# Optimization experiments

Measured on AMD Instinct MI355X. Metric: run time of the kernel, lower is better.

Reference implementation:

```python
import jax, jax.numpy as jnp
import numpy as np

N, E, KS, DIM = 6890, 41340, 5, 2
K = KS * KS  # 25 spline kernel buckets


def spline_conv(x, edge_index, pseudo, weight, root, bias):
    """Degree-1 open B-spline conv (SplineGCN), mean aggregation + root + bias.
    x: [N, Fin], weight: [K, Fin, Fout], root: [Fin, Fout], bias: [Fout]."""
    row, col = edge_index[0], edge_index[1]  # target, source
    pos = pseudo * (KS - 1)                   # [E, 2] in [0, KS-1]
    i0 = jnp.clip(jnp.floor(pos), 0, KS - 2).astype(jnp.int32)  # [E, 2]
    frac = pos - i0                           # [E, 2]
    # 4 nonzero basis products per edge (2 per dim)
    off = jnp.array([[0, 0], [1, 0], [0, 1], [1, 1]], dtype=jnp.int32)  # [4, 2]
    b_dim = jnp.stack([1.0 - frac, frac], axis=-1)  # [E, 2, 2] (dim, which-knot)
    w = b_dim[:, 0, off[:, 0]] * b_dim[:, 1, off[:, 1]]       # [E, 4]
    idx = (i0[:, None, 0] + off[None, :, 0]) + KS * (i0[:, None, 1] + off[None, :, 1])  # [E, 4]
    # transform all nodes by all K kernels once: [N, K, Fout]
    xw = jnp.einsum('ni,kio->nko', x, weight)
    g = xw[col[:, None], idx]                 # [E, 4, Fout] gather
    msg = jnp.einsum('es,eso->eo', w, g)      # [E, Fout]
    agg = jax.ops.segment_sum(msg, row, num_segments=N)
    deg = jax.ops.segment_sum(jnp.ones((E,), x.dtype), row, num_segments=N)
    agg = agg / jnp.maximum(deg, 1.0)[:, None]
    return agg + x @ root + bias


def setup_inputs() -> dict:
    key = jax.random.key(0)
    ks = jax.random.split(key, 20)
    def gl(k, shape):  # glorot-ish
        fan = shape[-2] if len(shape) > 1 else shape[-1]
        return jax.random.normal(k, shape, jnp.float32) / np.sqrt(fan)
    inp = {
        'x': jax.random.normal(ks[0], (N, 544), jnp.float32),
        'edge_index': jax.random.randint(ks[1], (2, E), 0, N),
        'pseudo': jax.random.uniform(ks[2], (E, DIM), jnp.float32),
        'W_lin': gl(ks[3], (544, 16)), 'b_lin': jnp.zeros((16,), jnp.float32),
        'w1': gl(ks[4], (K, 16, 32)),  'r1': gl(ks[5], (16, 32)),  'bi1': jnp.zeros((32,), jnp.float32),
        'w2': gl(ks[6], (K, 32, 64)),  'r2': gl(ks[7], (32, 64)),  'bi2': jnp.zeros((64,), jnp.float32),
        'w3': gl(ks[8], (K, 64, 128)), 'r3': gl(ks[9], (64, 128)), 'bi3': jnp.zeros((128,), jnp.float32),
        'W1': gl(ks[10], (128, 256)), 'b1': jnp.zeros((256,), jnp.float32),
        'W2': gl(ks[11], (256, 6890)), 'b2': jnp.zeros((6890,), jnp.float32),
    }
    return inp


def reference(x, edge_index, pseudo, W_lin, b_lin, w1, r1, bi1, w2, r2, bi2, w3, r3, bi3, W1, b1, W2, b2):
    h = jax.nn.elu(x @ W_lin + b_lin)
    h = jax.nn.elu(spline_conv(h, edge_index, pseudo, w1, r1, bi1))
    h = jax.nn.elu(spline_conv(h, edge_index, pseudo, w2, r2, bi2))
    h = jax.nn.elu(spline_conv(h, edge_index, pseudo, w3, r3, bi3))
    h = jax.nn.elu(h @ W1 + b1)
    # dropout is identity in eval mode
    logits = h @ W2 + b2
    return jax.nn.log_softmax(logits, axis=-1)
```

## Files before the change

### kernel.cpp

```cpp
#include <hip/hip_runtime.h>
#include <hip/hip_bf16.h>

#define NND 6890
#define NED 41340

typedef __bf16 bf16x8 __attribute__((ext_vector_type(8)));
typedef float f32x4 __attribute__((ext_vector_type(4)));
typedef unsigned short u16x4 __attribute__((ext_vector_type(4)));

__device__ inline unsigned short f32_bf16(float f) {
  unsigned int u = __float_as_uint(f);
  unsigned int r = (u + 0x7FFFu + ((u >> 16) & 1u)) >> 16;
  return (unsigned short)r;
}
__device__ inline void split2(float v, unsigned short& hi, unsigned short& lo) {
  unsigned short h = f32_bf16(v);
  float hf = __uint_as_float((unsigned int)h << 16);
  hi = h;
  lo = f32_bf16(v - hf);
}
__device__ inline float elu_f(float v) { return v > 0.f ? v : (expf(v) - 1.f); }

__device__ __forceinline__ void gload_lds16(const void* g, void* l) {
  __builtin_amdgcn_global_load_lds((const __attribute__((address_space(1))) void*)g,
                                   (__attribute__((address_space(3))) void*)l, 16, 0, 0);
}

__global__ void zero_int_kernel(int* p, int n) {
  int i = blockIdx.x * blockDim.x + threadIdx.x;
  if (i < n) p[i] = 0;
}

__global__ void edge_prep_kernel(const int* __restrict__ erow, const float* __restrict__ pseudo,
                                 float* __restrict__ ew, int* __restrict__ ek,
                                 int* __restrict__ deg, int E) {
  int e = blockIdx.x * blockDim.x + threadIdx.x;
  if (e >= E) return;
  float p0 = pseudo[2 * e + 0] * 4.0f;
  float p1 = pseudo[2 * e + 1] * 4.0f;
  int i0 = (int)floorf(p0); i0 = i0 < 0 ? 0 : (i0 > 3 ? 3 : i0);
  int i1 = (int)floorf(p1); i1 = i1 < 0 ? 0 : (i1 > 3 ? 3 : i1);
  float f0 = p0 - (float)i0, f1 = p1 - (float)i1;
  ew[4 * e + 0] = (1.f - f0) * (1.f - f1);
  ew[4 * e + 1] = f0 * (1.f - f1);
  ew[4 * e + 2] = (1.f - f0) * f1;
  ew[4 * e + 3] = f0 * f1;
  int b = i0 + 5 * i1;
  ek[4 * e + 0] = b; ek[4 * e + 1] = b + 1; ek[4 * e + 2] = b + 5; ek[4 * e + 3] = b + 6;
  atomicAdd(&deg[erow[e]], 1);
}

__global__ void scan_kernel(const int* __restrict__ deg, int* __restrict__ rowptr,
                            int* __restrict__ cursor, float* __restrict__ deginv, int n) {
  __shared__ int part[1024];
  int t = threadIdx.x;
  int CH = (n + 1023) >> 10;
  int base = t * CH;
  int s = 0;
  for (int j = 0; j < CH; ++j) { int i = base + j; if (i < n) s += deg[i]; }
  part[t] = s;
  __syncthreads();
  for (int off = 1; off < 1024; off <<= 1) {
    int v = (t >= off) ? part[t - off] : 0;
    __syncthreads();
    part[t] += v;
    __syncthreads();
  }
  int run = (t == 0) ? 0 : part[t - 1];
  for (int j = 0; j < CH; ++j) {
    int i = base + j;
    if (i < n) {
      rowptr[i] = run; cursor[i] = run;
      int d = deg[i];
      deginv[i] = 1.0f / fmaxf((float)d, 1.0f);
      run += d;
    }
  }
  if (t == 1023) rowptr[n] = part[1023];
}

__global__ void csr_fill_kernel(const int* __restrict__ erow, int* __restrict__ cursor,
                                int* __restrict__ csr, int E) {
  int e = blockIdx.x * blockDim.x + threadIdx.x;
  if (e >= E) return;
  int slot = atomicAdd(&cursor[erow[e]], 1);
  csr[slot] = e;
}

__global__ void split_kernel(const float* __restrict__ src, unsigned short* __restrict__ oh,
                             unsigned short* __restrict__ ol, int n4) {
  int i = blockIdx.x * 256 + threadIdx.x;
  if (i >= n4) return;
  f32x4 v = *(const f32x4*)(src + 4 * i);
  u16x4 h, l;
#pragma unroll
  for (int j = 0; j < 4; ++j) {
    unsigned short hh, ll;
    split2(v[j], hh, ll);
    h[j] = hh; l[j] = ll;
  }
  *(u16x4*)(oh + 4 * i) = h;
  *(u16x4*)(ol + 4 * i) = l;
}

__global__ void b_build_kernel(const float* __restrict__ x, const int* __restrict__ ecol,
                               const float* __restrict__ ew4, const int* __restrict__ ek4,
                               const int* __restrict__ rowptr, const int* __restrict__ csr,
                               const float* __restrict__ deginv,
                               unsigned short* __restrict__ Bh, unsigned short* __restrict__ Bl,
                               int Fin) {
  extern __shared__ float lds[];
  int r = blockIdx.x;
  int T = blockDim.x;
  int tid = threadIdx.x;
  int nb = 25 * Fin;
  int j = tid / Fin;
  int i = tid - j * Fin;
  float* plane = lds + j * nb;
  for (int t = tid; t < 4 * nb; t += T) lds[t] = 0.f;
  __syncthreads();
  int p0 = rowptr[r], p1 = rowptr[r + 1];
  for (int p = p0 + j; p < p1; p += 4) {
    int e = csr[p];
    int c = ecol[e];
    float xv = x[(size_t)c * Fin + i];
    f32x4 wv = *(const f32x4*)(ew4 + 4 * e);
    int4 kv = *(const int4*)(ek4 + 4 * e);
    plane[kv.x * Fin + i] += wv[0] * xv;
    plane[kv.y * Fin + i] += wv[1] * xv;
    plane[kv.z * Fin + i] += wv[2] * xv;
    plane[kv.w * Fin + i] += wv[3] * xv;
  }
  __syncthreads();
  float dinv = deginv[r];
  int tot = nb + Fin;
  for (int t = tid; t < tot; t += T) {
    float v;
    if (t < nb)
      v = (lds[t] + lds[nb + t] + lds[2 * nb + t] + lds[3 * nb + t]) * dinv;
    else
      v = x[(size_t)r * Fin + (t - nb)];
    unsigned short h, l;
    split2(v, h, l);
    Bh[(size_t)r * tot + t] = h;
    Bl[(size_t)r * tot + t] = l;
  }
}

__global__ void weights_prep_kernel(const float* __restrict__ W_lin, const float* __restrict__ w1,
                                    const float* __restrict__ r1, const float* __restrict__ w2,
                                    const float* __restrict__ r2, const float* __restrict__ w3,
                                    const float* __restrict__ r3, const float* __restrict__ W1,
                                    unsigned short* __restrict__ Th, unsigned short* __restrict__ Tl) {
  const int tstart[9] = {0, 17, 30, 31, 81, 83, 283, 291, 323};
  const int jK[8]    = {544, 400, 16, 800, 32, 1600, 64, 128};
  const int jF[8]    = {16, 32, 32, 64, 64, 128, 128, 256};
  const int jldt[8]  = {544, 416, 416, 832, 832, 1664, 1664, 128};
  const int jkoff[8] = {0, 0, 400, 0, 800, 0, 1600, 0};
  const int jdst[8]  = {0, 8704, 8704, 22016, 22016, 75264, 75264, 288256};
  int b = blockIdx.x;
  int job = 0;
  while (job < 7 && b >= tstart[job + 1]) ++job;
  int t = b - tstart[job];
  int fxc = (jF[job] + 31) >> 5;
  int kt = t / fxc, ft = t % fxc;
  const float* src;
  switch (job) {
    case 0: src = W_lin; break;
    case 1: src = w1; break;
    case 2: src = r1; break;
    case 3: src = w2; break;
    case 4: src = r2; break;
    case 5: src = w3; break;
    case 6: src = r3; break;
    default: src = W1; break;
  }
  int K = jK[job], F = jF[job], ldt = jldt[job], koff = jkoff[job];
  unsigned short* th = Th + jdst[job];
  unsigned short* tl = Tl + jdst[job];
  int k0 = kt * 32, c0 = ft * 32;
  __shared__ float tbuf[32][33];
  int tx = threadIdx.x & 31, ty = threadIdx.x >> 5;
  for (int j = ty; j < 32; j += 8) {
    int gk = k0 + j, gc = c0 + tx;
    tbuf[j][tx] = (gk < K && gc < F) ? src[(size_t)gk * F + gc] : 0.f;
  }
  __syncthreads();
  for (int j = ty; j < 32; j += 8) {
    int gc = c0 + j, gk = k0 + tx;
    if (gc < F && gk < K) {
      unsigned short h, lo2;
      split2(tbuf[tx][j], h, lo2);
      th[(size_t)gc * ldt + koff + gk] = h;
      tl[(size_t)gc * ldt + koff + gk] = lo2;
    }
  }
}

template <int BN>
__global__ __launch_bounds__(256) void gemm_x3_partial_kernel(
    const unsigned short* __restrict__ Ah, const unsigned short* __restrict__ Al,
    const unsigned short* __restrict__ Wh, const unsigned short* __restrict__ Wl,
    float* __restrict__ P, int M, int Kd, int F, int KS) {
  constexpr int AE = 64 * 32;
  constexpr int WE = BN * 32;
  __shared__ __align__(16) unsigned short lds[2][2 * AE + 2 * WE];
  int tid = threadIdx.x;
  int wave = tid >> 6, lane = tid & 63;
  int g = lane >> 4, r = lane & 15;
  int row0 = blockIdx.y * 64;
  int col0 = blockIdx.x * BN;
  int z = blockIdx.z;
  int nt = Kd >> 5;
  int ta = z * nt / KS, tb = (z + 1) * nt / KS;

  auto STAGE = [&](int buf, int kb) {
    {
      int rr = tid >> 2, pos = tid & 3;
      int c = (pos - rr) & 3;
      int gra = row0 + rr; if (gra >= M) gra = M - 1;
      size_t so = (size_t)gra * Kd + kb + c * 8;
      gload_lds16(Ah + so, &lds[buf][wave * 512]);
      gload_lds16(Al + so, &lds[buf][AE + wave * 512]);
    }
#pragma unroll
    for (int it = 0; it < (4 * BN + 255) / 256; ++it) {
      int idx = it * 256 + tid;
      if (idx < 4 * BN) {
        int rr = idx >> 2, pos = idx & 3;
        int c = (pos - rr) & 3;
        size_t so = (size_t)(col0 + rr) * Kd + kb + c * 8;
        gload_lds16(Wh + so, &lds[buf][2 * AE + (it * 256 + wave * 64) * 8]);
        gload_lds16(Wl + so, &lds[buf][2 * AE + WE + (it * 256 + wave * 64) * 8]);
      }
    }
  };

  constexpr int NF = BN / 16;
  f32x4 acc[NF];
#pragma unroll
  for (int n = 0; n < NF; ++n)
#pragma unroll
    for (int q = 0; q < 4; ++q) acc[n][q] = 0.f;

  int n = tb - ta;
  int rA = wave * 16 + r;
  int aoff = rA * 32 + ((g + rA) & 3) * 8;

  STAGE(0, ta * 32);
  __syncthreads();
  for (int tt = 0; tt < n; ++tt) {
    int buf = tt & 1;
    if (tt + 1 < n) STAGE(buf ^ 1, (ta + tt + 1) * 32);
    bf16x8 fah = *(const bf16x8*)&lds[buf][aoff];
    bf16x8 fal = *(const bf16x8*)&lds[buf][AE + aoff];
#pragma unroll
    for (int nn = 0; nn < NF; ++nn) {
      int rW = nn * 16 + r;
      int woff = rW * 32 + ((g + rW) & 3) * 8;
      bf16x8 fbh = *(const bf16x8*)&lds[buf][2 * AE + woff];
      bf16x8 fbl = *(const bf16x8*)&lds[buf][2 * AE + WE + woff];
      acc[nn] = __builtin_amdgcn_mfma_f32_16x16x32_bf16(fah, fbh, acc[nn], 0, 0, 0);
      acc[nn] = __builtin_amdgcn_mfma_f32_16x16x32_bf16(fal, fbh, acc[nn], 0, 0, 0);
      acc[nn] = __builtin_amdgcn_mfma_f32_16x16x32_bf16(fah, fbl, acc[nn], 0, 0, 0);
    }
    __syncthreads();
  }
#pragma unroll
  for (int nn = 0; nn < NF; ++nn) {
    int gc = col0 + nn * 16 + r;
#pragma unroll
    for (int q = 0; q < 4; ++q) {
      int gr = row0 + wave * 16 + g * 4 + q;
      if (gr < M) P[((size_t)z * M + gr) * F + gc] = acc[nn][q];
    }
  }
}

__global__ __launch_bounds__(256) void combine_elu_kernel(
    const float* __restrict__ P, const float* __restrict__ bias,
    float* __restrict__ outF, unsigned short* __restrict__ outB,
    unsigned short* __restrict__ outH, unsigned short* __restrict__ outL,
    int M, int F, int KS) {
  int i4 = blockIdx.x * 256 + threadIdx.x;
  int fv = F >> 2;
  int total = M * fv;
  if (i4 >= total) return;
  int gr = i4 / fv, c4 = (i4 - gr * fv) * 4;
  f32x4 s = {0.f, 0.f, 0.f, 0.f};
  for (int z = 0; z < KS; ++z)
    s += *(const f32x4*)(P + ((size_t)z * M + gr) * F + c4);
  f32x4 bv = *(const f32x4*)(bias + c4);
#pragma unroll
  for (int j = 0; j < 4; ++j) s[j] = elu_f(s[j] + bv[j]);
  if (outH) {
    u16x4 h, l;
#pragma unroll
    for (int j = 0; j < 4; ++j) {
      unsigned short hh, ll;
      split2(s[j], hh, ll);
      h[j] = hh; l[j] = ll;
    }
    *(u16x4*)(outH + (size_t)gr * F + c4) = h;
    *(u16x4*)(outL + (size_t)gr * F + c4) = l;
  } else if (outB) {
    u16x4 o;
#pragma unroll
    for (int j = 0; j < 4; ++j) o[j] = f32_bf16(s[j]);
    *(u16x4*)(outB + (size_t)gr * F + c4) = o;
  } else {
    *(f32x4*)(outF + (size_t)gr * F + c4) = s;
  }
}

__global__ void w2_cast_transpose_kernel(const float* __restrict__ W2,
                                         unsigned short* __restrict__ Wt, int K, int N) {
  __shared__ float t[32][33];
  int c0 = blockIdx.x * 32, k0 = blockIdx.y * 32;
  int tx = threadIdx.x, ty = threadIdx.y;
  for (int j = ty; j < 32; j += 8) {
    int gk = k0 + j, gc = c0 + tx;
    t[j][tx] = (gk < K && gc < N) ? W2[(size_t)gk * N + gc] : 0.f;
  }
  __syncthreads();
  for (int j = ty; j < 32; j += 8) {
    int gc = c0 + j, gk = k0 + tx;
    if (gc < N && gk < K) Wt[(size_t)gc * K + gk] = f32_bf16(t[tx][j]);
  }
}

template <int MODE>
__global__ __launch_bounds__(256) void gemm_final_kernel(
    const unsigned short* __restrict__ A, const unsigned short* __restrict__ Bt,
    const float* __restrict__ bias, const float* __restrict__ lse,
    float* __restrict__ outp, int M, int N) {
  __shared__ __align__(16) unsigned short lds[2][2][8192];
  int tid = threadIdx.x;
  int w = tid >> 6, l = tid & 63;
  int row0 = blockIdx.y * 128, col0 = blockIdx.x * 128;

  auto STAGE = [&](int buf, int kb) {
#pragma unroll
    for (int it = 0; it < 4; ++it) {
      int idx = it * 256 + tid;
      int rr = idx >> 3, pos = idx & 7;
      int c = (pos - rr) & 7;
      int gra = row0 + rr; if (gra >= M) gra = M - 1;
      int grb = col0 + rr; if (grb >= N) grb = N - 1;
      gload_lds16(A + (size_t)gra * 256 + kb + c * 8, &lds[buf][0][(it * 256 + w * 64) * 8]);
      gload_lds16(Bt + (size_t)grb * 256 + kb + c * 8, &lds[buf][1][(it * 256 + w * 64) * 8]);
    }
  };

  int wm = w >> 1, wn = w & 1;
  int g = l >> 4, r = l & 15;

  f32x4 acc[4][4];
#pragma unroll
  for (int mi = 0; mi < 4; ++mi)
#pragma unroll
    for (int ni = 0; ni < 4; ++ni)
#pragma unroll
      for (int q = 0; q < 4; ++q) acc[mi][ni][q] = 0.f;

  STAGE(0, 0);
  __syncthreads();
#pragma unroll
  for (int ks = 0; ks < 4; ++ks) {
    int buf = ks & 1;
    if (ks < 3) STAGE(buf ^ 1, (ks + 1) * 64);
#pragma unroll
    for (int sub = 0; sub < 2; ++sub) {
      bf16x8 fa[4], fb[4];
#pragma unroll
      for (int mi = 0; mi < 4; ++mi) {
        int rA = wm * 64 + mi * 16 + r;
        fa[mi] = *(const bf16x8*)&lds[buf][0][rA * 64 + ((g + 4 * sub + rA) & 7) * 8];
      }
#pragma unroll
      for (int ni = 0; ni < 4; ++ni) {
        int rB = wn * 64 + ni * 16 + r;
        fb[ni] = *(const bf16x8*)&lds[buf][1][rB * 64 + ((g + 4 * sub + rB) & 7) * 8];
      }
#pragma unroll
      for (int mi = 0; mi < 4; ++mi)
#pragma unroll
        for (int ni = 0; ni < 4; ++ni)
          acc[mi][ni] = __builtin_amdgcn_mfma_f32_16x16x32_bf16(fb[ni], fa[mi], acc[mi][ni], 0, 0, 0);
    }
    __syncthreads();
  }

  if (MODE == 0) {
    float bb[4][4];
#pragma unroll
    for (int ni = 0; ni < 4; ++ni) {
      int gc0 = col0 + wn * 64 + ni * 16 + g * 4;
#pragma unroll
      for (int q = 0; q < 4; ++q)
        bb[ni][q] = (gc0 + q < N) ? bias[gc0 + q] : 0.f;
    }
#pragma unroll
    for (int mi = 0; mi < 4; ++mi) {
      int gr = row0 + wm * 64 + mi * 16 + r;
      float vv[4][4];
      float mloc = -3e38f;
#pragma unroll
      for (int ni = 0; ni < 4; ++ni) {
        int gc0 = col0 + wn * 64 + ni * 16 + g * 4;
#pragma unroll
        for (int q = 0; q < 4; ++q) {
          float v = (gc0 + q < N) ? (acc[mi][ni][q] + bb[ni][q]) : -3e38f;
          vv[ni][q] = v;
          mloc = fmaxf(mloc, v);
        }
      }
      float sloc = 0.f;
#pragma unroll
      for (int ni = 0; ni < 4; ++ni) {
        int gc0 = col0 + wn * 64 + ni * 16 + g * 4;
#pragma unroll
        for (int q = 0; q < 4; ++q)
          if (gc0 + q < N) sloc += __expf(vv[ni][q] - mloc);
      }
#pragma unroll
      for (int off = 16; off < 64; off <<= 1) {
        float mo = __shfl_xor(mloc, off);
        float so = __shfl_xor(sloc, off);
        float mn = fmaxf(mloc, mo);
        sloc = sloc * __expf(mloc - mn) + so * __expf(mo - mn);
        mloc = mn;
      }
      if (g == 0 && gr < M) {
        int hb = blockIdx.x * 2 + wn;
        *(float2*)(outp + 2 * ((size_t)hb * M + gr)) = make_float2(mloc, sloc);
      }
    }
  } else {
    float* fsc = (float*)&lds[0][0][0];
    float* wbase = fsc + w * 4096;
#pragma unroll
    for (int mi = 0; mi < 4; ++mi) {
      int rr = mi * 16 + r;
#pragma unroll
      for (int ni = 0; ni < 4; ++ni) {
        int u = (ni * 4 + g + rr) & 15;
        *(f32x4*)(wbase + rr * 64 + u * 4) = acc[mi][ni];
      }
    }
    __syncthreads();
#pragma unroll
    for (int t = 0; t < 16; ++t) {
      int unit = t * 256 + tid;
      int rowi = unit >> 5, ch = unit & 31;
      int gr = row0 + rowi;
      if (gr >= M) continue;
      int reg = ((rowi >> 6) << 1) + (ch >> 4);
      int rr = rowi & 63;
      int u = ((ch & 15) + rr) & 15;
      f32x4 v = *(const f32x4*)(fsc + reg * 4096 + rr * 64 + u * 4);
      float L = lse[gr];
      int gc0 = col0 + ch * 4;
      if (gc0 + 4 <= N) {
        f32x4 bv = *(const f32x4*)(bias + gc0);
#pragma unroll
        for (int q = 0; q < 4; ++q) v[q] = v[q] + bv[q] - L;
        *(f32x4*)(outp + (size_t)gr * N + gc0) = v;
      } else {
#pragma unroll
        for (int q = 0; q < 4; ++q)
          if (gc0 + q < N) outp[(size_t)gr * N + gc0 + q] = v[q] + bias[gc0 + q] - L;
      }
    }
  }
}

__global__ __launch_bounds__(256) void lse_kernel(const float* __restrict__ stats,
                                                  float* __restrict__ lse, int M, int NH) {
  int row = blockIdx.x * 256 + threadIdx.x;
  if (row >= M) return;
  float m = -3e38f, s = 0.f;
  for (int hb = 0; hb < NH; ++hb) {
    float2 v = *(const float2*)(stats + 2 * ((size_t)hb * M + row));
    float mn = fmaxf(m, v.x);
    s = s * __expf(m - mn) + v.y * __expf(v.x - mn);
    m = mn;
  }
  lse[row] = m + logf(s);
}

extern "C" void kernel_launch(void* const* d_in, const int* in_sizes, int n_in,
                              void* d_out, int out_size, void* d_ws, size_t ws_size,
                              hipStream_t stream) {
  const int N = NND, E = NED;
  const float* x      = (const float*)d_in[0];
  const int*   ei     = (const int*)d_in[1];
  const float* pseudo = (const float*)d_in[2];
  const float* W_lin  = (const float*)d_in[3];
  const float* b_lin  = (const float*)d_in[4];
  const float* w1  = (const float*)d_in[5];
  const float* r1  = (const float*)d_in[6];
  const float* bi1 = (const float*)d_in[7];
  const float* w2  = (const float*)d_in[8];
  const float* r2  = (const float*)d_in[9];
  const float* bi2 = (const float*)d_in[10];
  const float* w3  = (const float*)d_in[11];
  const float* r3  = (const float*)d_in[12];
  const float* bi3 = (const float*)d_in[13];
  const float* W1  = (const float*)d_in[14];
  const float* b1  = (const float*)d_in[15];
  const float* W2  = (const float*)d_in[16];
  const float* b2  = (const float*)d_in[17];
  const int* erow = ei;
  const int* ecol = ei + E;

  char* scratch = (char*)d_out;
  size_t off = 0;
  auto alloc = [&](size_t bytes) -> void* {
    void* p = scratch + off;
    off = (off + bytes + 255) & ~(size_t)255;
    return p;
  };
  unsigned short* Bh = (unsigned short*)alloc((size_t)N * 1664 * 2);
  unsigned short* Bl = (unsigned short*)alloc((size_t)N * 1664 * 2);
  float* h0     = (float*)alloc((size_t)N * 16 * 4);
  float* h1     = (float*)alloc((size_t)N * 32 * 4);
  float* h2     = (float*)alloc((size_t)N * 64 * 4);
  unsigned short* h3h = (unsigned short*)alloc((size_t)N * 128 * 2);
  unsigned short* h3l = (unsigned short*)alloc((size_t)N * 128 * 2);
  unsigned short* xh  = (unsigned short*)alloc((size_t)N * 544 * 2);
  unsigned short* xl  = (unsigned short*)alloc((size_t)N * 544 * 2);
  unsigned short* Wth = (unsigned short*)alloc((size_t)321024 * 2);
  unsigned short* Wtl = (unsigned short*)alloc((size_t)321024 * 2);
  float* Pbuf   = (float*)alloc((size_t)4 * N * 128 * 4);
  float* stats  = (float*)alloc((size_t)108 * N * 2 * 4);
  float* ew     = (float*)alloc((size_t)E * 4 * 4);
  int*   ek     = (int*)alloc((size_t)E * 4 * 4);
  int*   deg    = (int*)alloc((size_t)N * 4);
  float* deginv = (float*)alloc((size_t)N * 4);
  int*   rowptr = (int*)alloc((size_t)(N + 1) * 4);
  int*   cursor = (int*)alloc((size_t)N * 4);
  int*   csr    = (int*)alloc((size_t)E * 4);

  unsigned short* h4b = (unsigned short*)d_ws;
  unsigned short* W2t = (unsigned short*)((char*)d_ws + (size_t)N * 256 * 2);
  float* lse = (float*)((char*)d_ws + (size_t)N * 256 * 4);

  zero_int_kernel<<<(N + 255) / 256, 256, 0, stream>>>(deg, N);
  edge_prep_kernel<<<(E + 255) / 256, 256, 0, stream>>>(erow, pseudo, ew, ek, deg, E);
  scan_kernel<<<1, 1024, 0, stream>>>(deg, rowptr, cursor, deginv, N);
  csr_fill_kernel<<<(E + 255) / 256, 256, 0, stream>>>(erow, cursor, csr, E);

  weights_prep_kernel<<<323, 256, 0, stream>>>(W_lin, w1, r1, w2, r2, w3, r3, W1, Wth, Wtl);
  split_kernel<<<(N * 136 + 255) / 256, 256, 0, stream>>>(x, xh, xl, N * 136);

  auto cgrid = [](int M_, int F_) { return dim3((M_ * (F_ / 4) + 255) / 256); };

  gemm_x3_partial_kernel<16><<<dim3(1, 108, 4), 256, 0, stream>>>(xh, xl, Wth + 0, Wtl + 0, Pbuf, N, 544, 16, 4);
  combine_elu_kernel<<<cgrid(N, 16), 256, 0, stream>>>(Pbuf, b_lin, h0, nullptr, nullptr, nullptr, N, 16, 4);

  b_build_kernel<<<N, 64, 4 * 25 * 16 * 4, stream>>>(h0, ecol, ew, ek, rowptr, csr, deginv, Bh, Bl, 16);
  gemm_x3_partial_kernel<32><<<dim3(1, 108, 4), 256, 0, stream>>>(Bh, Bl, Wth + 8704, Wtl + 8704, Pbuf, N, 416, 32, 4);
  combine_elu_kernel<<<cgrid(N, 32), 256, 0, stream>>>(Pbuf, bi1, h1, nullptr, nullptr, nullptr, N, 32, 4);

  b_build_kernel<<<N, 128, 4 * 25 * 32 * 4, stream>>>(h1, ecol, ew, ek, rowptr, csr, deginv, Bh, Bl, 32);
  gemm_x3_partial_kernel<64><<<dim3(1, 108, 4), 256, 0, stream>>>(Bh, Bl, Wth + 22016, Wtl + 22016, Pbuf, N, 832, 64, 4);
  combine_elu_kernel<<<cgrid(N, 64), 256, 0, stream>>>(Pbuf, bi2, h2, nullptr, nullptr, nullptr, N, 64, 4);

  b_build_kernel<<<N, 256, 4 * 25 * 64 * 4, stream>>>(h2, ecol, ew, ek, rowptr, csr, deginv, Bh, Bl, 64);
  gemm_x3_partial_kernel<128><<<dim3(1, 108, 4), 256, 0, stream>>>(Bh, Bl, Wth + 75264, Wtl + 75264, Pbuf, N, 1664, 128, 4);
  combine_elu_kernel<<<cgrid(N, 128), 256, 0, stream>>>(Pbuf, bi3, nullptr, nullptr, h3h, h3l, N, 128, 4);

  gemm_x3_partial_kernel<128><<<dim3(2, 108, 2), 256, 0, stream>>>(h3h, h3l, Wth + 288256, Wtl + 288256, Pbuf, N, 128, 256, 2);
  combine_elu_kernel<<<cgrid(N, 256), 256, 0, stream>>>(Pbuf, b1, nullptr, h4b, nullptr, nullptr, N, 256, 2);

  w2_cast_transpose_kernel<<<dim3(216, 8), dim3(32, 8), 0, stream>>>(W2, W2t, 256, N);

  gemm_final_kernel<0><<<dim3(54, 54), 256, 0, stream>>>(h4b, W2t, b2, nullptr, stats, N, N);

  lse_kernel<<<(N + 255) / 256, 256, 0, stream>>>(stats, lse, N, 108);

  gemm_final_kernel<1><<<dim3(54, 54), 256, 0, stream>>>(h4b, W2t, b2, lse, (float*)d_out, N, N);

  (void)in_sizes; (void)n_in; (void)out_size; (void)ws_size;
}
```

Before: 315.5 us.

## Fuse all stages into one cooperative persistent mega-kernel with grid syncs

New measurement: 901.9 us. 186% more time.

```diff
diff --git a/kernel.cpp b/kernel.cpp
--- a/kernel.cpp
+++ b/kernel.cpp
@@ -1,5 +1,8 @@
 #include <hip/hip_runtime.h>
 #include <hip/hip_bf16.h>
+#include <hip/hip_cooperative_groups.h>
+
+namespace cg = cooperative_groups;
 
 #define NND 6890
 #define NED 41340
@@ -26,561 +29,589 @@
                                    (__attribute__((address_space(3))) void*)l, 16, 0, 0);
 }
 
-__global__ void zero_int_kernel(int* p, int n) {
-  int i = blockIdx.x * blockDim.x + threadIdx.x;
-  if (i < n) p[i] = 0;
-}
-
-__global__ void edge_prep_kernel(const int* __restrict__ erow, const float* __restrict__ pseudo,
-                                 float* __restrict__ ew, int* __restrict__ ek,
-                                 int* __restrict__ deg, int E) {
-  int e = blockIdx.x * blockDim.x + threadIdx.x;
-  if (e >= E) return;
-  float p0 = pseudo[2 * e + 0] * 4.0f;
-  float p1 = pseudo[2 * e + 1] * 4.0f;
-  int i0 = (int)floorf(p0); i0 = i0 < 0 ? 0 : (i0 > 3 ? 3 : i0);
-  int i1 = (int)floorf(p1); i1 = i1 < 0 ? 0 : (i1 > 3 ? 3 : i1);
-  float f0 = p0 - (float)i0, f1 = p1 - (float)i1;
-  ew[4 * e + 0] = (1.f - f0) * (1.f - f1);
-  ew[4 * e + 1] = f0 * (1.f - f1);
-  ew[4 * e + 2] = (1.f - f0) * f1;
-  ew[4 * e + 3] = f0 * f1;
-  int b = i0 + 5 * i1;
-  ek[4 * e + 0] = b; ek[4 * e + 1] = b + 1; ek[4 * e + 2] = b + 5; ek[4 * e + 3] = b + 6;
-  atomicAdd(&deg[erow[e]], 1);
-}
-
-__global__ void scan_kernel(const int* __restrict__ deg, int* __restrict__ rowptr,
-                            int* __restrict__ cursor, float* __restrict__ deginv, int n) {
-  __shared__ int part[1024];
-  int t = threadIdx.x;
-  int CH = (n + 1023) >> 10;
-  int base = t * CH;
-  int s = 0;
-  for (int j = 0; j < CH; ++j) { int i = base + j; if (i < n) s += deg[i]; }
-  part[t] = s;
-  __syncthreads();
-  for (int off = 1; off < 1024; off <<= 1) {
-    int v = (t >= off) ? part[t - off] : 0;
-    __syncthreads();
-    part[t] += v;
-    __syncthreads();
-  }
-  int run = (t == 0) ? 0 : part[t - 1];
-  for (int j = 0; j < CH; ++j) {
-    int i = base + j;
-    if (i < n) {
-      rowptr[i] = run; cursor[i] = run;
-      int d = deg[i];
-      deginv[i] = 1.0f / fmaxf((float)d, 1.0f);
-      run += d;
-    }
-  }
-  if (t == 1023) rowptr[n] = part[1023];
-}
-
-__global__ void csr_fill_kernel(const int* __restrict__ erow, int* __restrict__ cursor,
-                                int* __restrict__ csr, int E) {
-  int e = blockIdx.x * blockDim.x + threadIdx.x;
-  if (e >= E) return;
-  int slot = atomicAdd(&cursor[erow[e]], 1);
-  csr[slot] = e;
-}
-
-__global__ void split_kernel(const float* __restrict__ src, unsigned short* __restrict__ oh,
-                             unsigned short* __restrict__ ol, int n4) {
-  int i = blockIdx.x * 256 + threadIdx.x;
-  if (i >= n4) return;
-  f32x4 v = *(const f32x4*)(src + 4 * i);
-  u16x4 h, l;
-#pragma unroll
-  for (int j = 0; j < 4; ++j) {
-    unsigned short hh, ll;
-    split2(v[j], hh, ll);
-    h[j] = hh; l[j] = ll;
-  }
-  *(u16x4*)(oh + 4 * i) = h;
-  *(u16x4*)(ol + 4 * i) = l;
-}
-
-__global__ void b_build_kernel(const float* __restrict__ x, const int* __restrict__ ecol,
-                               const float* __restrict__ ew4, const int* __restrict__ ek4,
-                               const int* __restrict__ rowptr, const int* __restrict__ csr,
-                               const float* __restrict__ deginv,
-                               unsigned short* __restrict__ Bh, unsigned short* __restrict__ Bl,
-                               int Fin) {
-  extern __shared__ float lds[];
-  int r = blockIdx.x;
-  int T = blockDim.x;
-  int tid = threadIdx.x;
-  int nb = 25 * Fin;
-  int j = tid / Fin;
-  int i = tid - j * Fin;
-  float* plane = lds + j * nb;
-  for (int t = tid; t < 4 * nb; t += T) lds[t] = 0.f;
-  __syncthreads();
-  int p0 = rowptr[r], p1 = rowptr[r + 1];
-  for (int p = p0 + j; p < p1; p += 4) {
-    int e = csr[p];
-    int c = ecol[e];
-    float xv = x[(size_t)c * Fin + i];
-    f32x4 wv = *(const f32x4*)(ew4 + 4 * e);
-    int4 kv = *(const int4*)(ek4 + 4 * e);
-    plane[kv.x * Fin + i] += wv[0] * xv;
-    plane[kv.y * Fin + i] += wv[1] * xv;
-    plane[kv.z * Fin + i] += wv[2] * xv;
-    plane[kv.w * Fin + i] += wv[3] * xv;
-  }
-  __syncthreads();
-  float dinv = deginv[r];
-  int tot = nb + Fin;
-  for (int t = tid; t < tot; t += T) {
-    float v;
-    if (t < nb)
-      v = (lds[t] + lds[nb + t] + lds[2 * nb + t] + lds[3 * nb + t]) * dinv;
-    else
-      v = x[(size_t)r * Fin + (t - nb)];
-    unsigned short h, l;
-    split2(v, h, l);
-    Bh[(size_t)r * tot + t] = h;
-    Bl[(size_t)r * tot + t] = l;
-  }
-}
-
-__global__ void weights_prep_kernel(const float* __restrict__ W_lin, const float* __restrict__ w1,
-                                    const float* __restrict__ r1, const float* __restrict__ w2,
-                                    const float* __restrict__ r2, const float* __restrict__ w3,
-                                    const float* __restrict__ r3, const float* __restrict__ W1,
-                                    unsigned short* __restrict__ Th, unsigned short* __restrict__ Tl) {
-  const int tstart[9] = {0, 17, 30, 31, 81, 83, 283, 291, 323};
-  const int jK[8]    = {544, 400, 16, 800, 32, 1600, 64, 128};
-  const int jF[8]    = {16, 32, 32, 64, 64, 128, 128, 256};
-  const int jldt[8]  = {544, 416, 416, 832, 832, 1664, 1664, 128};
-  const int jkoff[8] = {0, 0, 400, 0, 800, 0, 1600, 0};
-  const int jdst[8]  = {0, 8704, 8704, 22016, 22016, 75264, 75264, 288256};
-  int b = blockIdx.x;
-  int job = 0;
-  while (job < 7 && b >= tstart[job + 1]) ++job;
-  int t = b - tstart[job];
-  int fxc = (jF[job] + 31) >> 5;
-  int kt = t / fxc, ft = t % fxc;
-  const float* src;
-  switch (job) {
-    case 0: src = W_lin; break;
-    case 1: src = w1; break;
-    case 2: src = r1; break;
-    case 3: src = w2; break;
-    case 4: src = r2; break;
-    case 5: src = w3; break;
-    case 6: src = r3; break;
-    default: src = W1; break;
-  }
-  int K = jK[job], F = jF[job], ldt = jldt[job], koff = jkoff[job];
-  unsigned short* th = Th + jdst[job];
-  unsigned short* tl = Tl + jdst[job];
-  int k0 = kt * 32, c0 = ft * 32;
-  __shared__ float tbuf[32][33];
-  int tx = threadIdx.x & 31, ty = threadIdx.x >> 5;
-  for (int j = ty; j < 32; j += 8) {
-    int gk = k0 + j, gc = c0 + tx;
-    tbuf[j][tx] = (gk < K && gc < F) ? src[(size_t)gk * F + gc] : 0.f;
-  }
-  __syncthreads();
-  for (int j = ty; j < 32; j += 8) {
-    int gc = c0 + j, gk = k0 + tx;
-    if (gc < F && gk < K) {
-      unsigned short h, lo2;
-      split2(tbuf[tx][j], h, lo2);
-      th[(size_t)gc * ldt + koff + gk] = h;
-      tl[(size_t)gc * ldt + koff + gk] = lo2;
-    }
-  }
-}
-
-template <int BN>
-__global__ __launch_bounds__(256) void gemm_x3_partial_kernel(
-    const unsigned short* __restrict__ Ah, const unsigned short* __restrict__ Al,
-    const unsigned short* __restrict__ Wh, const unsigned short* __restrict__ Wl,
-    float* __restrict__ P, int M, int Kd, int F, int KS) {
+struct MP {
+  const float *x, *pseudo, *W_lin, *b_lin, *w1, *r1, *bi1, *w2, *r2, *bi2;
+  const float *w3, *r3, *bi3, *W1, *b1, *W2, *b2;
+  const int* ei;
+  unsigned short *Bh, *Bl, *h3h, *h3l, *xh, *xl, *Wth, *Wtl, *h4b, *W2t;
+  float *h0, *h1, *h2, *Pbuf, *stats, *ew, *deginv, *lse, *outp;
+  int *ek, *deg, *rowptr, *cursor, *csr;
+};
+
+__device__ void prep_tile(char* smem, const MP& p, int b, int tid) {
+  if (b < 323) {
+    const int tstart[9] = {0, 17, 30, 31, 81, 83, 283, 291, 323};
+    const int jK[8]    = {544, 400, 16, 800, 32, 1600, 64, 128};
+    const int jF[8]    = {16, 32, 32, 64, 64, 128, 128, 256};
+    const int jldt[8]  = {544, 416, 416, 832, 832, 1664, 1664, 128};
+    const int jkoff[8] = {0, 0, 400, 0, 800, 0, 1600, 0};
+    const int jdst[8]  = {0, 8704, 8704, 22016, 22016, 75264, 75264, 288256};
+    int job = 0;
+    while (job < 7 && b >= tstart[job + 1]) ++job;
+    int t = b - tstart[job];
+    int fxc = (jF[job] + 31) >> 5;
+    int kt = t / fxc, ft = t % fxc;
+    const float* src;
+    switch (job) {
+      case 0: src = p.W_lin; break;
+      case 1: src = p.w1; break;
+      case 2: src = p.r1; break;
+      case 3: src = p.w2; break;
+      case 4: src = p.r2; break;
+      case 5: src = p.w3; break;
+      case 6: src = p.r3; break;
+      default: src = p.W1; break;
+    }
+    int K = jK[job], F = jF[job], ldt = jldt[job], koff = jkoff[job];
+    unsigned short* th = p.Wth + jdst[job];
+    unsigned short* tl = p.Wtl + jdst[job];
+    int k0 = kt * 32, c0 = ft * 32;
+    float (*tbuf)[33] = (float(*)[33])smem;
+    int tx = tid & 31, ty = tid >> 5;
+    for (int j = ty; j < 32; j += 8) {
+      int gk = k0 + j, gc = c0 + tx;
+      tbuf[j][tx] = (gk < K && gc < F) ? src[(size_t)gk * F + gc] : 0.f;
+    }
+    __syncthreads();
+    for (int j = ty; j < 32; j += 8) {
+      int gc = c0 + j, gk = k0 + tx;
+      if (gc < F && gk < K) {
+        unsigned short h, lo2;
+        split2(tbuf[tx][j], h, lo2);
+        th[(size_t)gc * ldt + koff + gk] = h;
+        tl[(size_t)gc * ldt + koff + gk] = lo2;
+      }
+    }
+  } else if (b < 3984) {
+    int i = (b - 323) * 256 + tid;
+    if (i < NND * 136) {
+      f32x4 v = *(const f32x4*)(p.x + 4 * (size_t)i);
+      u16x4 h, l;
+#pragma unroll
+      for (int j = 0; j < 4; ++j) {
+        unsigned short hh, ll;
+        split2(v[j], hh, ll);
+        h[j] = hh; l[j] = ll;
+      }
+      *(u16x4*)(p.xh + 4 * (size_t)i) = h;
+      *(u16x4*)(p.xl + 4 * (size_t)i) = l;
+    }
+  } else {
+    int t = b - 3984;
+    int c0 = (t % 216) * 32, k0 = (t / 216) * 32;
+    float (*tbuf)[33] = (float(*)[33])smem;
+    int tx = tid & 31, ty = tid >> 5;
+    for (int j = ty; j < 32; j += 8) {
+      int gk = k0 + j, gc = c0 + tx;
+      tbuf[j][tx] = (gk < 256 && gc < NND) ? p.W2[(size_t)gk * NND + gc] : 0.f;
+    }
+    __syncthreads();
+    for (int j = ty; j < 32; j += 8) {
+      int gc = c0 + j, gk = k0 + tx;
+      if (gc < NND && gk < 256) p.W2t[(size_t)gc * 256 + gk] = f32_bf16(tbuf[tx][j]);
+    }
+  }
+}
+
+template <int BN, int OM>
+__device__ void mid_gemm(char* smem, const unsigned short* Ah, const unsigned short* Al,
+                         const unsigned short* Wh, const unsigned short* Wl,
+                         const float* bias, float* outF, unsigned short* outB, float* P,
+                         int Kd, int F, int KS, int bid, int nbk, int tid) {
   constexpr int AE = 64 * 32;
   constexpr int WE = BN * 32;
-  __shared__ __align__(16) unsigned short lds[2][2 * AE + 2 * WE];
-  int tid = threadIdx.x;
+  constexpr int NF = BN / 16;
+  constexpr int BUFSZ = 2 * AE + 2 * WE;
+  unsigned short* ldsbase = (unsigned short*)smem;
   int wave = tid >> 6, lane = tid & 63;
   int g = lane >> 4, r = lane & 15;
-  int row0 = blockIdx.y * 64;
-  int col0 = blockIdx.x * BN;
-  int z = blockIdx.z;
+  const int gy = (NND + 63) >> 6;
+  const int gx = F / BN;
   int nt = Kd >> 5;
-  int ta = z * nt / KS, tb = (z + 1) * nt / KS;
-
-  auto STAGE = [&](int buf, int kb) {
-    {
-      int rr = tid >> 2, pos = tid & 3;
-      int c = (pos - rr) & 3;
-      int gra = row0 + rr; if (gra >= M) gra = M - 1;
-      size_t so = (size_t)gra * Kd + kb + c * 8;
-      gload_lds16(Ah + so, &lds[buf][wave * 512]);
-      gload_lds16(Al + so, &lds[buf][AE + wave * 512]);
-    }
-#pragma unroll
-    for (int it = 0; it < (4 * BN + 255) / 256; ++it) {
-      int idx = it * 256 + tid;
-      if (idx < 4 * BN) {
-        int rr = idx >> 2, pos = idx & 3;
-        int c = (pos - rr) & 3;
-        size_t so = (size_t)(col0 + rr) * Kd + kb + c * 8;
-        gload_lds16(Wh + so, &lds[buf][2 * AE + (it * 256 + wave * 64) * 8]);
-        gload_lds16(Wl + so, &lds[buf][2 * AE + WE + (it * 256 + wave * 64) * 8]);
-      }
-    }
-  };
-
-  constexpr int NF = BN / 16;
-  f32x4 acc[NF];
-#pragma unroll
-  for (int n = 0; n < NF; ++n)
-#pragma unroll
-    for (int q = 0; q < 4; ++q) acc[n][q] = 0.f;
-
-  int n = tb - ta;
+  int ntiles = gx * gy * KS;
   int rA = wave * 16 + r;
   int aoff = rA * 32 + ((g + rA) & 3) * 8;
 
-  STAGE(0, ta * 32);
-  __syncthreads();
-  for (int tt = 0; tt < n; ++tt) {
-    int buf = tt & 1;
-    if (tt + 1 < n) STAGE(buf ^ 1, (ta + tt + 1) * 32);
-    bf16x8 fah = *(const bf16x8*)&lds[buf][aoff];
-    bf16x8 fal = *(const bf16x8*)&lds[buf][AE + aoff];
+  for (int t = bid; t < ntiles; t += nbk) {
+    int z = t / (gx * gy);
+    int rem = t - z * (gx * gy);
+    int by = rem / gx, bx = rem - by * gx;
+    int row0 = by * 64, col0 = bx * BN;
+    int ta = z * nt / KS, tb = (z + 1) * nt / KS;
+    int n = tb - ta;
+
+    auto STAGE = [&](int buf, int kb) {
+      unsigned short* lds = ldsbase + buf * BUFSZ;
+      {
+        int rr = tid >> 2, pos = tid & 3;
+        int c = (pos - rr) & 3;
+        int gra = row0 + rr; if (gra >= NND) gra = NND - 1;
+        size_t so = (size_t)gra * Kd + kb + c * 8;
+        gload_lds16(Ah + so, lds + wave * 512);
+        gload_lds16(Al + so, lds + AE + wave * 512);
+      }
+#pragma unroll
+      for (int it = 0; it < (4 * BN + 255) / 256; ++it) {
+        int idx = it * 256 + tid;
+        if (idx < 4 * BN) {
+          int rr = idx >> 2, pos = idx & 3;
+          int c = (pos - rr) & 3;
+          size_t so = (size_t)(col0 + rr) * Kd + kb + c * 8;
+          gload_lds16(Wh + so, lds + 2 * AE + (it * 256 + wave * 64) * 8);
+          gload_lds16(Wl + so, lds + 2 * AE + WE + (it * 256 + wave * 64) * 8);
+        }
+      }
+    };
+
+    f32x4 acc[NF];
+#pragma unroll
+    for (int nn = 0; nn < NF; ++nn)
+#pragma unroll
+      for (int q = 0; q < 4; ++q) acc[nn][q] = 0.f;
+
+    STAGE(0, ta * 32);
+    __syncthreads();
+    for (int tt = 0; tt < n; ++tt) {
+      int buf = tt & 1;
+      if (tt + 1 < n) STAGE(buf ^ 1, (ta + tt + 1) * 32);
+      unsigned short* lds = ldsbase + buf * BUFSZ;
+      bf16x8 fah = *(const bf16x8*)(lds + aoff);
+      bf16x8 fal = *(const bf16x8*)(lds + AE + aoff);
+#pragma unroll
+      for (int nn = 0; nn < NF; ++nn) {
+        int rW = nn * 16 + r;
+        int woff = rW * 32 + ((g + rW) & 3) * 8;
+        bf16x8 fbh = *(const bf16x8*)(lds + 2 * AE + woff);
+        bf16x8 fbl = *(const bf16x8*)(lds + 2 * AE + WE + woff);
+        acc[nn] = __builtin_amdgcn_mfma_f32_16x16x32_bf16(fah, fbh, acc[nn], 0, 0, 0);
+        acc[nn] = __builtin_amdgcn_mfma_f32_16x16x32_bf16(fal, fbh, acc[nn], 0, 0, 0);
+        acc[nn] = __builtin_amdgcn_mfma_f32_16x16x32_bf16(fah, fbl, acc[nn], 0, 0, 0);
+      }
+      __syncthreads();
+    }
 #pragma unroll
     for (int nn = 0; nn < NF; ++nn) {
-      int rW = nn * 16 + r;
-      int woff = rW * 32 + ((g + rW) & 3) * 8;
-      bf16x8 fbh = *(const bf16x8*)&lds[buf][2 * AE + woff];
-      bf16x8 fbl = *(const bf16x8*)&lds[buf][2 * AE + WE + woff];
-      acc[nn] = __builtin_amdgcn_mfma_f32_16x16x32_bf16(fah, fbh, acc[nn], 0, 0, 0);
-      acc[nn] = __builtin_amdgcn_mfma_f32_16x16x32_bf16(fal, fbh, acc[nn], 0, 0, 0);
-      acc[nn] = __builtin_amdgcn_mfma_f32_16x16x32_bf16(fah, fbl, acc[nn], 0, 0, 0);
-    }
-    __syncthreads();
-  }
-#pragma unroll
-  for (int nn = 0; nn < NF; ++nn) {
-    int gc = col0 + nn * 16 + r;
-#pragma unroll
-    for (int q = 0; q < 4; ++q) {
-      int gr = row0 + wave * 16 + g * 4 + q;
-      if (gr < M) P[((size_t)z * M + gr) * F + gc] = acc[nn][q];
-    }
-  }
-}
-
-__global__ __launch_bounds__(256) void combine_elu_kernel(
-    const float* __restrict__ P, const float* __restrict__ bias,
-    float* __restrict__ outF, unsigned short* __restrict__ outB,
-    unsigned short* __restrict__ outH, unsigned short* __restrict__ outL,
-    int M, int F, int KS) {
-  int i4 = blockIdx.x * 256 + threadIdx.x;
+      int gc = col0 + nn * 16 + r;
+      float bv = (OM == 3) ? 0.f : bias[gc];
+#pragma unroll
+      for (int q = 0; q < 4; ++q) {
+        int gr = row0 + wave * 16 + g * 4 + q;
+        if (gr < NND) {
+          if (OM == 3) {
+            P[((size_t)z * NND + gr) * F + gc] = acc[nn][q];
+          } else {
+            float v = elu_f(acc[nn][q] + bv);
+            if (OM == 0) outF[(size_t)gr * F + gc] = v;
+            else outB[(size_t)gr * F + gc] = f32_bf16(v);
+          }
+        }
+      }
+    }
+  }
+}
+
+__device__ void combine_phase(const float* P, const float* bias, float* outF,
+                              unsigned short* outH, unsigned short* outL,
+                              int F, int KS, int gidx, int gstride) {
   int fv = F >> 2;
-  int total = M * fv;
-  if (i4 >= total) return;
-  int gr = i4 / fv, c4 = (i4 - gr * fv) * 4;
-  f32x4 s = {0.f, 0.f, 0.f, 0.f};
-  for (int z = 0; z < KS; ++z)
-    s += *(const f32x4*)(P + ((size_t)z * M + gr) * F + c4);
-  f32x4 bv = *(const f32x4*)(bias + c4);
-#pragma unroll
-  for (int j = 0; j < 4; ++j) s[j] = elu_f(s[j] + bv[j]);
-  if (outH) {
-    u16x4 h, l;
-#pragma unroll
-    for (int j = 0; j < 4; ++j) {
-      unsigned short hh, ll;
-      split2(s[j], hh, ll);
-      h[j] = hh; l[j] = ll;
-    }
-    *(u16x4*)(outH + (size_t)gr * F + c4) = h;
-    *(u16x4*)(outL + (size_t)gr * F + c4) = l;
-  } else if (outB) {
-    u16x4 o;
-#pragma unroll
-    for (int j = 0; j < 4; ++j) o[j] = f32_bf16(s[j]);
-    *(u16x4*)(outB + (size_t)gr * F + c4) = o;
-  } else {
-    *(f32x4*)(outF + (size_t)gr * F + c4) = s;
-  }
-}
-
-__global__ void w2_cast_transpose_kernel(const float* __restrict__ W2,
-                                         unsigned short* __restrict__ Wt, int K, int N) {
-  __shared__ float t[32][33];
-  int c0 = blockIdx.x * 32, k0 = blockIdx.y * 32;
-  int tx = threadIdx.x, ty = threadIdx.y;
-  for (int j = ty; j < 32; j += 8) {
-    int gk = k0 + j, gc = c0 + tx;
-    t[j][tx] = (gk < K && gc < N) ? W2[(size_t)gk * N + gc] : 0.f;
-  }
-  __syncthreads();
-  for (int j = ty; j < 32; j += 8) {
-    int gc = c0 + j, gk = k0 + tx;
-    if (gc < N && gk < K) Wt[(size_t)gc * K + gk] = f32_bf16(t[tx][j]);
+  int total = NND * fv;
+  for (int i4 = gidx; i4 < total; i4 += gstride) {
+    int gr = i4 / fv, c4 = (i4 - gr * fv) * 4;
+    f32x4 s = {0.f, 0.f, 0.f, 0.f};
+    for (int z = 0; z < KS; ++z)
+      s += *(const f32x4*)(P + ((size_t)z * NND + gr) * F + c4);
+    f32x4 bv = *(const f32x4*)(bias + c4);
+#pragma unroll
+    for (int j = 0; j < 4; ++j) s[j] = elu_f(s[j] + bv[j]);
+    if (outH) {
+      u16x4 h, l;
+#pragma unroll
+      for (int j = 0; j < 4; ++j) {
+        unsigned short hh, ll;
+        split2(s[j], hh, ll);
+        h[j] = hh; l[j] = ll;
+      }
+      *(u16x4*)(outH + (size_t)gr * F + c4) = h;
+      *(u16x4*)(outL + (size_t)gr * F + c4) = l;
+    } else {
+      *(f32x4*)(outF + (size_t)gr * F + c4) = s;
+    }
+  }
+}
+
+__device__ void b_build_phase(char* smem, const float* x, const int* ecol,
+                              const float* ew4, const int* ek4, const int* rowptr,
+                              const int* csr, const float* deginv,
+                              unsigned short* Bh, unsigned short* Bl,
+                              int Fin, int bid, int nbk, int tid) {
+  float* lds = (float*)smem;
+  int nb4 = 25 * Fin;
+  int tpr = 4 * Fin;
+  int rpb = 256 / tpr;
+  int group = tid / tpr;
+  int t2 = tid - group * tpr;
+  int j = t2 / Fin, i = t2 - j * Fin;
+  float* plane = lds + (group * 4 + j) * nb4;
+  int nrt = (NND + rpb - 1) / rpb;
+  for (int rt = bid; rt < nrt; rt += nbk) {
+    int r = rt * rpb + group;
+    for (int tt = tid; tt < 4 * nb4 * rpb; tt += 256) lds[tt] = 0.f;
+    __syncthreads();
+    if (r < NND) {
+      int p0 = rowptr[r], p1 = rowptr[r + 1];
+      for (int p = p0 + j; p < p1; p += 4) {
+        int e = csr[p];
+        int c = ecol[e];
+        float xv = x[(size_t)c * Fin + i];
+        f32x4 wv = *(const f32x4*)(ew4 + 4 * e);
+        int4 kv = *(const int4*)(ek4 + 4 * e);
+        plane[kv.x * Fin + i] += wv[0] * xv;
+        plane[kv.y * Fin + i] += wv[1] * xv;
+        plane[kv.z * Fin + i] += wv[2] * xv;
+        plane[kv.w * Fin + i] += wv[3] * xv;
+      }
+    }
+    __syncthreads();
+    if (r < NND) {
+      float dinv = deginv[r];
+      int tot = 26 * Fin;
+      float* base = lds + group * 4 * nb4;
+      for (int tt = t2; tt < tot; tt += tpr) {
+        float v;
+        if (tt < nb4)
+          v = (base[tt] + base[nb4 + tt] + base[2 * nb4 + tt] + base[3 * nb4 + tt]) * dinv;
+        else
+          v = x[(size_t)r * Fin + (tt - nb4)];
+        unsigned short h, l;
+        split2(v, h, l);
+        Bh[(size_t)r * tot + tt] = h;
+        Bl[(size_t)r * tot + tt] = l;
+      }
+    }
+    __syncthreads();
   }
 }
 
 template <int MODE>
-__global__ __launch_bounds__(256) void gemm_final_kernel(
-    const unsigned short* __restrict__ A, const unsigned short* __restrict__ Bt,
-    const float* __restrict__ bias, const float* __restrict__ lse,
-    float* __restrict__ outp, int M, int N) {
-  __shared__ __align__(16) unsigned short lds[2][2][8192];
-  int tid = threadIdx.x;
+__device__ void final_gemm(char* smem, const unsigned short* A, const unsigned short* Bt,
+                           const float* bias, const float* lsep, float* outp,
+                           int bid, int nbk, int tid) {
+  const int M = NND, N = NND;
+  auto lds = reinterpret_cast<unsigned short(*)[2][8192]>(smem);
   int w = tid >> 6, l = tid & 63;
-  int row0 = blockIdx.y * 128, col0 = blockIdx.x * 128;
-
-  auto STAGE = [&](int buf, int kb) {
-#pragma unroll
-    for (int it = 0; it < 4; ++it) {
-      int idx = it * 256 + tid;
-      int rr = idx >> 3, pos = idx & 7;
-      int c = (pos - rr) & 7;
-      int gra = row0 + rr; if (gra >= M) gra = M - 1;
-      int grb = col0 + rr; if (grb >= N) grb = N - 1;
-      gload_lds16(A + (size_t)gra * 256 + kb + c * 8, &lds[buf][0][(it * 256 + w * 64) * 8]);
-      gload_lds16(Bt + (size_t)grb * 256 + kb + c * 8, &lds[buf][1][(it * 256 + w * 64) * 8]);
-    }
-  };
-
   int wm = w >> 1, wn = w & 1;
   int g = l >> 4, r = l & 15;
 
-  f32x4 acc[4][4];
-#pragma unroll
-  for (int mi = 0; mi < 4; ++mi)
-#pragma unroll
-    for (int ni = 0; ni < 4; ++ni)
-#pragma unroll
-      for (int q = 0; q < 4; ++q) acc[mi][ni][q] = 0.f;
-
-  STAGE(0, 0);
-  __syncthreads();
-#pragma unroll
-  for (int ks = 0; ks < 4; ++ks) {
-    int buf = ks & 1;
-    if (ks < 3) STAGE(buf ^ 1, (ks + 1) * 64);
-#pragma unroll
-    for (int sub = 0; sub < 2; ++sub) {
-      bf16x8 fa[4], fb[4];
-#pragma unroll
-      for (int mi = 0; mi < 4; ++mi) {
-        int rA = wm * 64 + mi * 16 + r;
-        fa[mi] = *(const bf16x8*)&lds[buf][0][rA * 64 + ((g + 4 * sub + rA) & 7) * 8];
-      }
-#pragma unroll
-      for (int ni = 0; ni < 4; ++ni) {
-        int rB = wn * 64 + ni * 16 + r;
-        fb[ni] = *(const bf16x8*)&lds[buf][1][rB * 64 + ((g + 4 * sub + rB) & 7) * 8];
-      }
-#pragma unroll
-      for (int mi = 0; mi < 4; ++mi)
-#pragma unroll
-        for (int ni = 0; ni < 4; ++ni)
-          acc[mi][ni] = __builtin_amdgcn_mfma_f32_16x16x32_bf16(fb[ni], fa[mi], acc[mi][ni], 0, 0, 0);
-    }
-    __syncthreads();
-  }
-
-  if (MODE == 0) {
-    float bb[4][4];
-#pragma unroll
-    for (int ni = 0; ni < 4; ++ni) {
-      int gc0 = col0 + wn * 64 + ni * 16 + g * 4;
-#pragma unroll
-      for (int q = 0; q < 4; ++q)
-        bb[ni][q] = (gc0 + q < N) ? bias[gc0 + q] : 0.f;
-    }
-#pragma unroll
-    for (int mi = 0; mi < 4; ++mi) {
-      int gr = row0 + wm * 64 + mi * 16 + r;
-      float vv[4][4];
-      float mloc = -3e38f;
+  for (int t0 = bid; t0 < 54 * 54; t0 += nbk) {
+    int by = t0 / 54, bx = t0 - by * 54;
+    int row0 = by * 128, col0 = bx * 128;
+
+    auto STAGE = [&](int buf, int kb) {
+#pragma unroll
+      for (int it = 0; it < 4; ++it) {
+        int idx = it * 256 + tid;
+        int rr = idx >> 3, pos = idx & 7;
+        int c = (pos - rr) & 7;
+        int gra = row0 + rr; if (gra >= M) gra = M - 1;
+        int grb = col0 + rr; if (grb >= N) grb = N - 1;
+        gload_lds16(A + (size_t)gra * 256 + kb + c * 8, &lds[buf][0][(it * 256 + w * 64) * 8]);
+        gload_lds16(Bt + (size_t)grb * 256 + kb + c * 8, &lds[buf][1][(it * 256 + w * 64) * 8]);
+      }
+    };
+
+    f32x4 acc[4][4];
+#pragma unroll
+    for (int mi = 0; mi < 4; ++mi)
+#pragma unroll
+      for (int ni = 0; ni < 4; ++ni)
+#pragma unroll
+        for (int q = 0; q < 4; ++q) acc[mi][ni][q] = 0.f;
+
+    STAGE(0, 0);
+    __syncthreads();
+#pragma unroll
+    for (int ks = 0; ks < 4; ++ks) {
+      int buf = ks & 1;
+      if (ks < 3) STAGE(buf ^ 1, (ks + 1) * 64);
+#pragma unroll
+      for (int sub = 0; sub < 2; ++sub) {
+        bf16x8 fa[4], fb[4];
+#pragma unroll
+        for (int mi = 0; mi < 4; ++mi) {
+          int rAi = wm * 64 + mi * 16 + r;
+          fa[mi] = *(const bf16x8*)&lds[buf][0][rAi * 64 + ((g + 4 * sub + rAi) & 7) * 8];
+        }
+#pragma unroll
+        for (int ni = 0; ni < 4; ++ni) {
+          int rBi = wn * 64 + ni * 16 + r;
+          fb[ni] = *(const bf16x8*)&lds[buf][1][rBi * 64 + ((g + 4 * sub + rBi) & 7) * 8];
+        }
+#pragma unroll
+        for (int mi = 0; mi < 4; ++mi)
+#pragma unroll
+          for (int ni = 0; ni < 4; ++ni)
+            acc[mi][ni] = __builtin_amdgcn_mfma_f32_16x16x32_bf16(fb[ni], fa[mi], acc[mi][ni], 0, 0, 0);
+      }
+      __syncthreads();
+    }
+
+    if (MODE == 0) {
+      float bb[4][4];
 #pragma unroll
       for (int ni = 0; ni < 4; ++ni) {
         int gc0 = col0 + wn * 64 + ni * 16 + g * 4;
 #pragma unroll
-        for (int q = 0; q < 4; ++q) {
-          float v = (gc0 + q < N) ? (acc[mi][ni][q] + bb[ni][q]) : -3e38f;
-          vv[ni][q] = v;
-          mloc = fmaxf(mloc, v);
-        }
-      }
-      float sloc = 0.f;
-#pragma unroll
-      for (int ni = 0; ni < 4; ++ni) {
-        int gc0 = col0 + wn * 64 + ni * 16 + g * 4;
-#pragma unroll
         for (int q = 0; q < 4; ++q)
-          if (gc0 + q < N) sloc += __expf(vv[ni][q] - mloc);
-      }
-#pragma unroll
-      for (int off = 16; off < 64; off <<= 1) {
-        float mo = __shfl_xor(mloc, off);
-        float so = __shfl_xor(sloc, off);
-        float mn = fmaxf(mloc, mo);
-        sloc = sloc * __expf(mloc - mn) + so * __expf(mo - mn);
-        mloc = mn;
-      }
-      if (g == 0 && gr < M) {
-        int hb = blockIdx.x * 2 + wn;
-        *(float2*)(outp + 2 * ((size_t)hb * M + gr)) = make_float2(mloc, sloc);
-      }
-    }
+          bb[ni][q] = (gc0 + q < N) ? bias[gc0 + q] : 0.f;
+      }
+#pragma unroll
+      for (int mi = 0; mi < 4; ++mi) {
+        int gr = row0 + wm * 64 + mi * 16 + r;
+        float vv[4][4];
+        float mloc = -3e38f;
+#pragma unroll
+        for (int ni = 0; ni < 4; ++ni) {
+          int gc0 = col0 + wn * 64 + ni * 16 + g * 4;
+#pragma unroll
+          for (int q = 0; q < 4; ++q) {
+            float v = (gc0 + q < N) ? (acc[mi][ni][q] + bb[ni][q]) : -3e38f;
+            vv[ni][q] = v;
+            mloc = fmaxf(mloc, v);
+          }
+        }
+        float sloc = 0.f;
+#pragma unroll
+        for (int ni = 0; ni < 4; ++ni) {
+          int gc0 = col0 + wn * 64 + ni * 16 + g * 4;
+#pragma unroll
+          for (int q = 0; q < 4; ++q)
+            if (gc0 + q < N) sloc += __expf(vv[ni][q] - mloc);
+        }
+#pragma unroll
+        for (int off = 16; off < 64; off <<= 1) {
+          float mo = __shfl_xor(mloc, off);
+          float so = __shfl_xor(sloc, off);
+          float mn = fmaxf(mloc, mo);
+          sloc = sloc * __expf(mloc - mn) + so * __expf(mo - mn);
+          mloc = mn;
+        }
+        if (g == 0 && gr < M) {
+          int hb = bx * 2 + wn;
+          *(float2*)(outp + 2 * ((size_t)hb * M + gr)) = make_float2(mloc, sloc);
+        }
+      }
+    } else {
+      float* fsc = (float*)smem;
+      float* wbase = fsc + w * 4096;
+#pragma unroll
+      for (int mi = 0; mi < 4; ++mi) {
+        int rr = mi * 16 + r;
+#pragma unroll
+        for (int ni = 0; ni < 4; ++ni) {
+          int u = (ni * 4 + g + rr) & 15;
+          *(f32x4*)(wbase + rr * 64 + u * 4) = acc[mi][ni];
+        }
+      }
+      __syncthreads();
+#pragma unroll
+      for (int tt = 0; tt < 16; ++tt) {
+        int unit = tt * 256 + tid;
+        int rowi = unit >> 5, ch = unit & 31;
+        int gr = row0 + rowi;
+        if (gr < M) {
+          int reg = ((rowi >> 6) << 1) + (ch >> 4);
+          int rr = rowi & 63;
+          int u = ((ch & 15) + rr) & 15;
+          f32x4 v = *(const f32x4*)(fsc + reg * 4096 + rr * 64 + u * 4);
+          float L = lsep[gr];
+          int gc0 = col0 + ch * 4;
+          if (gc0 + 4 <= N) {
+            f32x4 bv = *(const f32x4*)(bias + gc0);
+#pragma unroll
+            for (int q = 0; q < 4; ++q) v[q] = v[q] + bv[q] - L;
+            *(f32x4*)(outp + (size_t)gr * N + gc0) = v;
+          } else {
+#pragma unroll
+            for (int q = 0; q < 4; ++q)
+              if (gc0 + q < N) outp[(size_t)gr * N + gc0 + q] = v[q] + bias[gc0 + q] - L;
+          }
+        }
+      }
+      __syncthreads();
+    }
+  }
+}
+
+__global__ __launch_bounds__(256, 2) void mega_kernel(MP p) {
+  cg::grid_group grid = cg::this_grid();
+  __shared__ __align__(16) char smem[65536];
+  const int bid = blockIdx.x;
+  const int nbk = gridDim.x;
+  const int tid = threadIdx.x;
+  const int gidx = bid * 256 + tid;
+  const int gstride = nbk * 256;
+  const int* erow = p.ei;
+  const int* ecol = p.ei + NED;
+
+  for (int i = gidx; i < NND; i += gstride) p.deg[i] = 0;
+  grid.sync();
+
+  for (int e = gidx; e < NED; e += gstride) {
+    float p0 = p.pseudo[2 * e + 0] * 4.0f;
+    float p1 = p.pseudo[2 * e + 1] * 4.0f;
+    int i0 = (int)floorf(p0); i0 = i0 < 0 ? 0 : (i0 > 3 ? 3 : i0);
+    int i1 = (int)floorf(p1); i1 = i1 < 0 ? 0 : (i1 > 3 ? 3 : i1);
+    float f0 = p0 - (float)i0, f1 = p1 - (float)i1;
+    p.ew[4 * e + 0] = (1.f - f0) * (1.f - f1);
+    p.ew[4 * e + 1] = f0 * (1.f - f1);
+    p.ew[4 * e + 2] = (1.f - f0) * f1;
+    p.ew[4 * e + 3] = f0 * f1;
+    int b = i0 + 5 * i1;
+    p.ek[4 * e + 0] = b; p.ek[4 * e + 1] = b + 1;
+    p.ek[4 * e + 2] = b + 5; p.ek[4 * e + 3] = b + 6;
+    atomicAdd(&p.deg[erow[e]], 1);
+  }
+  grid.sync();
+
+  if (bid == 0) {
+    int* part = (int*)smem;
+    const int CH = (NND + 255) >> 8;
+    int base = tid * CH;
+    int s = 0;
+    for (int j = 0; j < CH; ++j) { int i = base + j; if (i < NND) s += p.deg[i]; }
+    part[tid] = s;
+    __syncthreads();
+    for (int off = 1; off < 256; off <<= 1) {
+      int v = (tid >= off) ? part[tid - off] : 0;
+      __syncthreads();
+      part[tid] += v;
+      __syncthreads();
+    }
+    int run = (tid == 0) ? 0 : part[tid - 1];
+    for (int j = 0; j < CH; ++j) {
+      int i = base + j;
+      if (i < NND) {
+        p.rowptr[i] = run;
+        p.cursor[i] = run;
+        int d = p.deg[i];
+        p.deginv[i] = 1.0f / fmaxf((float)d, 1.0f);
+        run += d;
+      }
+    }
+    if (tid == 255) p.rowptr[NND] = part[255];
   } else {
-    float* fsc = (float*)&lds[0][0][0];
-    float* wbase = fsc + w * 4096;
-#pragma unroll
-    for (int mi = 0; mi < 4; ++mi) {
-      int rr = mi * 16 + r;
-#pragma unroll
-      for (int ni = 0; ni < 4; ++ni) {
-        int u = (ni * 4 + g + rr) & 15;
-        *(f32x4*)(wbase + rr * 64 + u * 4) = acc[mi][ni];
-      }
-    }
-    __syncthreads();
-#pragma unroll
-    for (int t = 0; t < 16; ++t) {
-      int unit = t * 256 + tid;
-      int rowi = unit >> 5, ch = unit & 31;
-      int gr = row0 + rowi;
-      if (gr >= M) continue;
-      int reg = ((rowi >> 6) << 1) + (ch >> 4);
-      int rr = rowi & 63;
-      int u = ((ch & 15) + rr) & 15;
-      f32x4 v = *(const f32x4*)(fsc + reg * 4096 + rr * 64 + u * 4);
-      float L = lse[gr];
-      int gc0 = col0 + ch * 4;
-      if (gc0 + 4 <= N) {
-        f32x4 bv = *(const f32x4*)(bias + gc0);
-#pragma unroll
-        for (int q = 0; q < 4; ++q) v[q] = v[q] + bv[q] - L;
-        *(f32x4*)(outp + (size_t)gr * N + gc0) = v;
-      } else {
-#pragma unroll
-        for (int q = 0; q < 4; ++q)
-          if (gc0 + q < N) outp[(size_t)gr * N + gc0 + q] = v[q] + bias[gc0 + q] - L;
-      }
-    }
-  }
-}
-
-__global__ __launch_bounds__(256) void lse_kernel(const float* __restrict__ stats,
-                                                  float* __restrict__ lse, int M, int NH) {
-  int row = blockIdx.x * 256 + threadIdx.x;
-  if (row >= M) return;
-  float m = -3e38f, s = 0.f;
-  for (int hb = 0; hb < NH; ++hb) {
-    float2 v = *(const float2*)(stats + 2 * ((size_t)hb * M + row));
-    float mn = fmaxf(m, v.x);
-    s = s * __expf(m - mn) + v.y * __expf(v.x - mn);
-    m = mn;
-  }
-  lse[row] = m + logf(s);
+    for (int vt = bid - 1; vt < 5712; vt += nbk - 1) {
+      prep_tile(smem, p, vt, tid);
+      __syncthreads();
+    }
+  }
+  grid.sync();
+
+  for (int e = gidx; e < NED; e += gstride) {
+    int slot = atomicAdd(&p.cursor[erow[e]], 1);
+    p.csr[slot] = e;
+  }
+  grid.sync();
+
+  mid_gemm<16, 0>(smem, p.xh, p.xl, p.Wth, p.Wtl, p.b_lin, p.h0, nullptr, nullptr,
+                  544, 16, 1, bid, nbk, tid);
+  grid.sync();
+  b_build_phase(smem, p.h0, ecol, p.ew, p.ek, p.rowptr, p.csr, p.deginv, p.Bh, p.Bl,
+                16, bid, nbk, tid);
+  grid.sync();
+  mid_gemm<32, 0>(smem, p.Bh, p.Bl, p.Wth + 8704, p.Wtl + 8704, p.bi1, p.h1, nullptr, nullptr,
+                  416, 32, 1, bid, nbk, tid);
+  grid.sync();
+  b_build_phase(smem, p.h1, ecol, p.ew, p.ek, p.rowptr, p.csr, p.deginv, p.Bh, p.Bl,
+                32, bid, nbk, tid);
+  grid.sync();
+  mid_gemm<64, 3>(smem, p.Bh, p.Bl, p.Wth + 22016, p.Wtl + 22016, nullptr, nullptr, nullptr,
+                  p.Pbuf, 832, 64, 4, bid, nbk, tid);
+  grid.sync();
+  combine_phase(p.Pbuf, p.bi2, p.h2, nullptr, nullptr, 64, 4, gidx, gstride);
+  grid.sync();
+  b_build_phase(smem, p.h2, ecol, p.ew, p.ek, p.rowptr, p.csr, p.deginv, p.Bh, p.Bl,
+                64, bid, nbk, tid);
+  grid.sync();
+  mid_gemm<128, 3>(smem, p.Bh, p.Bl, p.Wth + 75264, p.Wtl + 75264, nullptr, nullptr, nullptr,
+                   p.Pbuf, 1664, 128, 4, bid, nbk, tid);
+  grid.sync();
+  combine_phase(p.Pbuf, p.bi3, nullptr, p.h3h, p.h3l, 128, 4, gidx, gstride);
+  grid.sync();
+  mid_gemm<128, 2>(smem, p.h3h, p.h3l, p.Wth + 288256, p.Wtl + 288256, p.b1, nullptr, p.h4b,
+                   nullptr, 128, 256, 1, bid, nbk, tid);
+  grid.sync();
+  final_gemm<0>(smem, p.h4b, p.W2t, p.b2, nullptr, p.stats, bid, nbk, tid);
+  grid.sync();
+  for (int row = gidx; row < NND; row += gstride) {
+    float m = -3e38f, s = 0.f;
+    for (int hb = 0; hb < 108; ++hb) {
+      float2 v = *(const float2*)(p.stats + 2 * ((size_t)hb * NND + row));
+      float mn = fmaxf(m, v.x);
+      s = s * __expf(m - mn) + v.y * __expf(v.x - mn);
+      m = mn;
+    }
+    p.lse[row] = m + logf(s);
+  }
+  grid.sync();
+  final_gemm<1>(smem, p.h4b, p.W2t, p.b2, p.lse, p.outp, bid, nbk, tid);
 }
 
 extern "C" void kernel_launch(void* const* d_in, const int* in_sizes, int n_in,
                               void* d_out, int out_size, void* d_ws, size_t ws_size,
                               hipStream_t stream) {
-  const int N = NND, E = NED;
-  const float* x      = (const float*)d_in[0];
-  const int*   ei     = (const int*)d_in[1];
-  const float* pseudo = (const float*)d_in[2];
-  const float* W_lin  = (const float*)d_in[3];
-  const float* b_lin  = (const float*)d_in[4];
-  const float* w1  = (const float*)d_in[5];
-  const float* r1  = (const float*)d_in[6];
-  const float* bi1 = (const float*)d_in[7];
-  const float* w2  = (const float*)d_in[8];
-  const float* r2  = (const float*)d_in[9];
-  const float* bi2 = (const float*)d_in[10];
-  const float* w3  = (const float*)d_in[11];
-  const float* r3  = (const float*)d_in[12];
-  const float* bi3 = (const float*)d_in[13];
-  const float* W1  = (const float*)d_in[14];
-  const float* b1  = (const float*)d_in[15];
-  const float* W2  = (const float*)d_in[16];
-  const float* b2  = (const float*)d_in[17];
-  const int* erow = ei;
-  const int* ecol = ei + E;
+  MP p;
+  p.x      = (const float*)d_in[0];
+  p.ei     = (const int*)d_in[1];
+  p.pseudo = (const float*)d_in[2];
+  p.W_lin  = (const float*)d_in[3];
+  p.b_lin  = (const float*)d_in[4];
+  p.w1  = (const float*)d_in[5];  p.r1 = (const float*)d_in[6];  p.bi1 = (const float*)d_in[7];
+  p.w2  = (const float*)d_in[8];  p.r2 = (const float*)d_in[9];  p.bi2 = (const float*)d_in[10];
+  p.w3  = (const float*)d_in[11]; p.r3 = (const float*)d_in[12]; p.bi3 = (const float*)d_in[13];
+  p.W1  = (const float*)d_in[14]; p.b1 = (const float*)d_in[15];
+  p.W2  = (const float*)d_in[16]; p.b2 = (const float*)d_in[17];
 
   char* scratch = (char*)d_out;
   size_t off = 0;
   auto alloc = [&](size_t bytes) -> void* {
-    void* p = scratch + off;
+    void* q = scratch + off;
     off = (off + bytes + 255) & ~(size_t)255;
-    return p;
+    return q;
   };
-  unsigned short* Bh = (unsigned short*)alloc((size_t)N * 1664 * 2);
-  unsigned short* Bl = (unsigned short*)alloc((size_t)N * 1664 * 2);
-  float* h0     = (float*)alloc((size_t)N * 16 * 4);
-  float* h1     = (float*)alloc((size_t)N * 32 * 4);
-  float* h2     = (float*)alloc((size_t)N * 64 * 4);
-  unsigned short* h3h = (unsigned short*)alloc((size_t)N * 128 * 2);
-  unsigned short* h3l = (unsigned short*)alloc((size_t)N * 128 * 2);
-  unsigned short* xh  = (unsigned short*)alloc((size_t)N * 544 * 2);
-  unsigned short* xl  = (unsigned short*)alloc((size_t)N * 544 * 2);
-  unsigned short* Wth = (unsigned short*)alloc((size_t)321024 * 2);
-  unsigned short* Wtl = (unsigned short*)alloc((size_t)321024 * 2);
-  float* Pbuf   = (float*)alloc((size_t)4 * N * 128 * 4);
-  float* stats  = (float*)alloc((size_t)108 * N * 2 * 4);
-  float* ew     = (float*)alloc((size_t)E * 4 * 4);
-  int*   ek     = (int*)alloc((size_t)E * 4 * 4);
-  int*   deg    = (int*)alloc((size_t)N * 4);
-  float* deginv = (float*)alloc((size_t)N * 4);
-  int*   rowptr = (int*)alloc((size_t)(N + 1) * 4);
-  int*   cursor = (int*)alloc((size_t)N * 4);
-  int*   csr    = (int*)alloc((size_t)E * 4);
-
-  unsigned short* h4b = (unsigned short*)d_ws;
-  unsigned short* W2t = (unsigned short*)((char*)d_ws + (size_t)N * 256 * 2);
-  float* lse = (float*)((char*)d_ws + (size_t)N * 256 * 4);
-
-  zero_int_kernel<<<(N + 255) / 256, 256, 0, stream>>>(deg, N);
-  edge_prep_kernel<<<(E + 255) / 256, 256, 0, stream>>>(erow, pseudo, ew, ek, deg, E);
-  scan_kernel<<<1, 1024, 0, stream>>>(deg, rowptr, cursor, deginv, N);
-  csr_fill_kernel<<<(E + 255) / 256, 256, 0, stream>>>(erow, cursor, csr, E);
-
-  weights_prep_kernel<<<323, 256, 0, stream>>>(W_lin, w1, r1, w2, r2, w3, r3, W1, Wth, Wtl);
-  split_kernel<<<(N * 136 + 255) / 256, 256, 0, stream>>>(x, xh, xl, N * 136);
-
-  auto cgrid = [](int M_, int F_) { return dim3((M_ * (F_ / 4) + 255) / 256); };
-
-  gemm_x3_partial_kernel<16><<<dim3(1, 108, 4), 256, 0, stream>>>(xh, xl, Wth + 0, Wtl + 0, Pbuf, N, 544, 16, 4);
-  combine_elu_kernel<<<cgrid(N, 16), 256, 0, stream>>>(Pbuf, b_lin, h0, nullptr, nullptr, nullptr, N, 16, 4);
-
-  b_build_kernel<<<N, 64, 4 * 25 * 16 * 4, stream>>>(h0, ecol, ew, ek, rowptr, csr, deginv, Bh, Bl, 16);
-  gemm_x3_partial_kernel<32><<<dim3(1, 108, 4), 256, 0, stream>>>(Bh, Bl, Wth + 8704, Wtl + 8704, Pbuf, N, 416, 32, 4);
-  combine_elu_kernel<<<cgrid(N, 32), 256, 0, stream>>>(Pbuf, bi1, h1, nullptr, nullptr, nullptr, N, 32, 4);
-
-  b_build_kernel<<<N, 128, 4 * 25 * 32 * 4, stream>>>(h1, ecol, ew, ek, rowptr, csr, deginv, Bh, Bl, 32);
-  gemm_x3_partial_kernel<64><<<dim3(1, 108, 4), 256, 0, stream>>>(Bh, Bl, Wth + 22016, Wtl + 22016, Pbuf, N, 832, 64, 4);
-  combine_elu_kernel<<<cgrid(N, 64), 256, 0, stream>>>(Pbuf, bi2, h2, nullptr, nullptr, nullptr, N, 64, 4);
-
-  b_build_kernel<<<N, 256, 4 * 25 * 64 * 4, stream>>>(h2, ecol, ew, ek, rowptr, csr, deginv, Bh, Bl, 64);
-  gemm_x3_partial_kernel<128><<<dim3(1, 108, 4), 256, 0, stream>>>(Bh, Bl, Wth + 75264, Wtl + 75264, Pbuf, N, 1664, 128, 4);
-  combine_elu_kernel<<<cgrid(N, 128), 256, 0, stream>>>(Pbuf, bi3, nullptr, nullptr, h3h, h3l, N, 128, 4);
-
-  gemm_x3_partial_kernel<128><<<dim3(2, 108, 2), 256, 0, stream>>>(h3h, h3l, Wth + 288256, Wtl + 288256, Pbuf, N, 128, 256, 2);
-  combine_elu_kernel<<<cgrid(N, 256), 256, 0, stream>>>(Pbuf, b1, nullptr, h4b, nullptr, nullptr, N, 256, 2);
-
-  w2_cast_transpose_kernel<<<dim3(216, 8), dim3(32, 8), 0, stream>>>(W2, W2t, 256, N);
-
-  gemm_final_kernel<0><<<dim3(54, 54), 256, 0, stream>>>(h4b, W2t, b2, nullptr, stats, N, N);
-
-  lse_kernel<<<(N + 255) / 256, 256, 0, stream>>>(stats, lse, N, 108);
-
-  gemm_final_kernel<1><<<dim3(54, 54), 256, 0, stream>>>(h4b, W2t, b2, lse, (float*)d_out, N, N);
+  p.Bh  = (unsigned short*)alloc((size_t)NND * 1664 * 2);
+  p.Bl  = (unsigned short*)alloc((size_t)NND * 1664 * 2);
+  p.h0  = (float*)alloc((size_t)NND * 16 * 4);
+  p.h1  = (float*)alloc((size_t)NND * 32 * 4);
+  p.h2  = (float*)alloc((size_t)NND * 64 * 4);
+  p.h3h = (unsigned short*)alloc((size_t)NND * 128 * 2);
+  p.h3l = (unsigned short*)alloc((size_t)NND * 128 * 2);
+  p.xh  = (unsigned short*)alloc((size_t)NND * 544 * 2);
+  p.xl  = (unsigned short*)alloc((size_t)NND * 544 * 2);
+  p.Wth = (unsigned short*)alloc((size_t)321024 * 2);
+  p.Wtl = (unsigned short*)alloc((size_t)321024 * 2);
+  p.Pbuf  = (float*)alloc((size_t)4 * NND * 128 * 4);
+  p.stats = (float*)alloc((size_t)108 * NND * 2 * 4);
+  p.ew  = (float*)alloc((size_t)NED * 4 * 4);
+  p.ek  = (int*)alloc((size_t)NED * 4 * 4);
+  p.deg = (int*)alloc((size_t)NND * 4);
+  p.deginv = (float*)alloc((size_t)NND * 4);
+  p.rowptr = (int*)alloc((size_t)(NND + 1) * 4);
+  p.cursor = (int*)alloc((size_t)NND * 4);
+  p.csr = (int*)alloc((size_t)NED * 4);
+  p.outp = (float*)d_out;
+
+  p.h4b = (unsigned short*)d_ws;
+  p.W2t = (unsigned short*)((char*)d_ws + (size_t)NND * 256 * 2);
+  p.lse = (float*)((char*)d_ws + (size_t)NND * 256 * 4);
+
+  int occ = 0;
+  hipOccupancyMaxActiveBlocksPerMultiprocessor(&occ, (const void*)mega_kernel, 256, 0);
+  if (occ < 1) occ = 1;
+  if (occ > 2) occ = 2;
+  dim3 grid(occ * 256);
+  void* args[] = {(void*)&p};
+  hipLaunchCooperativeKernel((const void*)mega_kernel, grid, dim3(256), args, 0, stream);
 
   (void)in_sizes; (void)n_in; (void)out_size; (void)ws_size;
 }
```
